# Performance work log

Hardware: AMD Instinct MI355X
Metric: run time of the kernel (lower is better)

Reference implementation:

```python
import jax, jax.numpy as jnp
import numpy as np

EPS = 1e-5  # BatchNorm eps


def _bn(x, g, b, axes):
    # training-mode batch norm over `axes`, channel dim broadcast via g/b shape
    m = jnp.mean(x, axis=axes, keepdims=True)
    v = jnp.var(x, axis=axes, keepdims=True)
    shape = [1] * x.ndim
    ch_axis = [a for a in range(x.ndim) if a not in axes][0]
    shape[ch_axis] = g.shape[0]
    return g.reshape(shape) * (x - m) * jax.lax.rsqrt(v + EPS) + b.reshape(shape)


def setup_inputs() -> dict:
    key = jax.random.key(0)
    ks = jax.random.split(key, 8)
    B, C, N = 16, 3, 2048

    def w(k_, fan_in, fan_out):
        return jax.random.normal(k_, (fan_in, fan_out), jnp.float32) * (1.0 / np.sqrt(fan_in))

    return {
        "pc": jax.random.normal(ks[0], (B, C, N), jnp.float32),
        "W1": w(ks[1], 6, 64), "g1": jnp.ones(64), "b1": jnp.zeros(64),
        "W2": w(ks[2], 64, 128), "g2": jnp.ones(128), "b2": jnp.zeros(128),
        "W3": w(ks[3], 128, 1024), "g3": jnp.ones(1024), "b3": jnp.zeros(1024),
        "Wf1": w(ks[4], 1024, 512), "gf1": jnp.ones(512), "bf1": jnp.zeros(512),
        "Wf2": w(ks[5], 512, 256), "gf2": jnp.ones(256), "bf2": jnp.zeros(256),
        "Wf3": jnp.zeros((256, 9), jnp.float32),           # zero-initialized per source
        "bf3": jnp.eye(3, dtype=jnp.float32).reshape(-1),  # identity bias per source
        "k": 20,
    }


def reference(pc, W1, g1, b1, W2, g2, b2, W3, g3, b3,
              Wf1, gf1, bf1, Wf2, gf2, bf2, Wf3, bf3, k):
    B, C, N = pc.shape
    # ---- KNN graph on coordinates (B x C x N) ----
    sq = jnp.sum(pc * pc, axis=1)                      # B,N
    inner = jnp.einsum('bcn,bcm->bnm', pc, pc)         # B,N,N
    negdist = 2.0 * inner - sq[:, :, None] - sq[:, None, :]
    _, idx = jax.lax.top_k(negdist, k)                 # B,N,k (includes self)
    # gather neighbor features: f (C,N), i (N,k) -> (C,N,k)
    topk = jax.vmap(lambda f, i: f[:, i])(pc, idx)     # B,C,N,k
    center = pc[:, :, :, None]
    edge = jnp.concatenate(
        [jnp.broadcast_to(center, topk.shape), topk - center], axis=1)  # B,2C,N,k

    # ---- edge conv (1x1 conv + BN + ReLU), pool=False ----
    h = jnp.einsum('bcnk,co->bonk', edge, W1)
    h = jax.nn.relu(_bn(h, g1, b1, (0, 2, 3)))         # B,64,N,k
    # ---- conv2 then max over k ----
    h = jnp.einsum('bcnk,co->bonk', h, W2)
    h = jax.nn.relu(_bn(h, g2, b2, (0, 2, 3)))         # B,128,N,k
    h = jnp.max(h, axis=-1)                            # B,128,N
    # ---- conv3 then max over N ----
    h = jnp.einsum('bcn,co->bon', h, W3)
    h = jax.nn.relu(_bn(h, g3, b3, (0, 2)))            # B,1024,N
    h = jnp.max(h, axis=-1)                            # B,1024
    # ---- FC stack ----
    h = jax.nn.relu(_bn(h @ Wf1, gf1, bf1, (0,)))      # B,512
    h = jax.nn.relu(_bn(h @ Wf2, gf2, bf2, (0,)))      # B,256
    h = h @ Wf3 + bf3                                  # B,9
    return h.reshape(B, 3, 3)
```

## Files before the change

### kernel.cpp

```cpp
#include <hip/hip_runtime.h>
#include <math.h>

#define Nn 2048

#define OFF_IDX    ((size_t)0)
#define OFF_P2MAX  (((size_t)4)  << 20)
#define OFF_P2MIN  (((size_t)13) << 20)
#define OFF_PS2    (((size_t)22) << 20)
#define OFF_PQ2    (((size_t)23) << 20)
#define OFF_STATS  (((size_t)24) << 20)
#define OFF_MOM    (OFF_STATS + 0)
#define OFF_A2C2   (OFF_STATS + 8192)
#define OFF_S3SUM  (OFF_STATS + 12288)
#define OFF_S3SQ   (OFF_STATS + 20480)
#define OFF_P3MAX  (OFF_STATS + 28672)
#define OFF_P3MIN  (OFF_STATS + 94208)
#define OFF_DOTS1  (OFF_STATS + 274432)
#define OFF_DOTS2  (OFF_STATS + 307200)
#define OFF_W2BF   (OFF_STATS + 323584)
#define OFF_W3BF   (OFF_STATS + 339968)
#define WS_NEEDED  (OFF_STATS + 602112)

typedef __attribute__((ext_vector_type(8))) short bf16x8;
typedef __attribute__((ext_vector_type(4))) float f32x4;

__device__ __forceinline__ unsigned fkey(float f){
  unsigned u = __float_as_uint(f);
  return (u & 0x80000000u) ? ~u : (u | 0x80000000u);
}
__device__ __forceinline__ float fdec(unsigned k){
  unsigned u = (k & 0x80000000u) ? (k & 0x7FFFFFFFu) : ~k;
  return __uint_as_float(u);
}
__device__ __forceinline__ short f2bf(float x){
  unsigned u = __float_as_uint(x);
  u += 0x7fffu + ((u >> 16) & 1u);
  return (short)(u >> 16);
}
__device__ __forceinline__ float bf2f(short v){
  return __uint_as_float(((unsigned)(unsigned short)v) << 16);
}
__device__ __forceinline__ float med3(float a, float b, float c){
  float d;
  asm("v_med3_f32 %0, %1, %2, %3" : "=v"(d) : "v"(a), "v"(b), "v"(c));
  return d;
}
__device__ __forceinline__ float ndist(float tQx, float tQy, float tQz, float Qw, float4 P){
  return fmaf(tQx, P.x, fmaf(tQy, P.y, fmaf(tQz, P.z, -Qw - P.w)));
}
__device__ __forceinline__ void insert20(float (&m)[20], float x){
  #pragma unroll
  for (int t = 0; t < 19; t++) m[t] = med3(m[t], m[t+1], x);
  m[19] = fmaxf(m[19], x);
}

__global__ __launch_bounds__(256) void k_setup(char* __restrict__ ws,
      const float* __restrict__ W2, const float* __restrict__ W3,
      short* __restrict__ W2BF, short* __restrict__ W3BF){
  int i = blockIdx.x*256 + threadIdx.x;
  if (i < 7168) ((unsigned*)(ws + OFF_MOM))[i] = 0u;
  if (i < 16384){
    ((unsigned*)(ws + OFF_P3MAX))[i] = 0u;
    ((unsigned*)(ws + OFF_P3MIN))[i] = 0xFFFFFFFFu;
  }
  if (i < 12288) ((float*)(ws + OFF_DOTS1))[i] = 0.f;
  if (i < 16384){
    int q = i >> 4, k0 = (i & 15)*8;
    bf16x8 vv;
    #pragma unroll
    for (int j = 0; j < 8; j++) vv[j] = f2bf(W3[(size_t)(k0+j)*1024 + q]);
    *(bf16x8*)&W3BF[q*128 + k0] = vv;
  } else if (i < 17408){
    int id2 = i - 16384;
    int q = id2 >> 3, k0 = (id2 & 7)*8;
    bf16x8 vv;
    #pragma unroll
    for (int j = 0; j < 8; j++) vv[j] = f2bf(W2[(k0+j)*128 + q]);
    *(bf16x8*)&W2BF[q*64 + k0] = vv;
  }
}

__global__ __launch_bounds__(512) void k_knn(const float* __restrict__ pc,
                                             int* __restrict__ idxg,
                                             double* __restrict__ MOM){
  __shared__ float4 pts[Nn];
  __shared__ unsigned cnt[64];
  __shared__ float momS[27];
  const int tid = threadIdx.x;
  const int b = blockIdx.y;
  const int n0 = blockIdx.x*64;
  const float* pcb = pc + b*3*Nn;
  for (int i = tid; i < Nn; i += 512){
    float x = pcb[i], y = pcb[Nn+i], z = pcb[2*Nn+i];
    pts[i] = make_float4(x, y, z, x*x + y*y + z*z);
  }
  if (tid < 64) cnt[tid] = 0u;
  if (tid < 27) momS[tid] = 0.f;
  __syncthreads();

  const int ql = tid >> 3, c = tid & 7;
  const int n = n0 + ql;
  const float4 Q = pts[n];
  const float tQx = 2.f*Q.x, tQy = 2.f*Q.y, tQz = 2.f*Q.z;

  float v[20];
  #pragma unroll
  for (int t = 0; t < 20; t++) v[t] = -3.4e38f;
  #pragma unroll 1
  for (int i = 0; i < 256; i += 4){
    float4 P0 = pts[(i+0)*8 + c];
    float4 P1 = pts[(i+1)*8 + c];
    float4 P2 = pts[(i+2)*8 + c];
    float4 P3 = pts[(i+3)*8 + c];
    insert20(v, ndist(tQx, tQy, tQz, Q.w, P0));
    insert20(v, ndist(tQx, tQy, tQz, Q.w, P1));
    insert20(v, ndist(tQx, tQy, tQz, Q.w, P2));
    insert20(v, ndist(tQx, tQy, tQz, Q.w, P3));
  }

  #pragma unroll
  for (int stage = 4; stage >= 1; stage >>= 1){
    float w[20];
    #pragma unroll
    for (int t = 0; t < 20; t++) w[t] = __shfl_xor(v[t], stage);
    #pragma unroll
    for (int t = 0; t < 20; t++) insert20(v, w[t]);
  }
  const float th = v[0];

  int* myidx = &idxg[((size_t)((b<<11) + n))*20];
  #pragma unroll 1
  for (int i = 0; i < 256; i += 4){
    float4 P0 = pts[(i+0)*8 + c];
    float4 P1 = pts[(i+1)*8 + c];
    float4 P2 = pts[(i+2)*8 + c];
    float4 P3 = pts[(i+3)*8 + c];
    float nd0 = ndist(tQx, tQy, tQz, Q.w, P0);
    float nd1 = ndist(tQx, tQy, tQz, Q.w, P1);
    float nd2 = ndist(tQx, tQy, tQz, Q.w, P2);
    float nd3 = ndist(tQx, tQy, tQz, Q.w, P3);
    if (nd0 >= th){ unsigned p = atomicAdd(&cnt[ql], 1u); if (p < 20u) myidx[p] = (i+0)*8 + c; }
    if (nd1 >= th){ unsigned p = atomicAdd(&cnt[ql], 1u); if (p < 20u) myidx[p] = (i+1)*8 + c; }
    if (nd2 >= th){ unsigned p = atomicAdd(&cnt[ql], 1u); if (p < 20u) myidx[p] = (i+2)*8 + c; }
    if (nd3 >= th){ unsigned p = atomicAdd(&cnt[ql], 1u); if (p < 20u) myidx[p] = (i+3)*8 + c; }
  }
  __threadfence_block();
  __syncthreads();

  if (c == 0){
    unsigned have = cnt[ql]; if (have > 20u) have = 20u;
    for (unsigned p = have; p < 20u; ++p) myidx[p] = n;
  }
  __threadfence_block();
  __syncthreads();

  float s1[6] = {0,0,0,0,0,0};
  float s2[21] = {0,0,0,0,0,0,0,0,0,0,0,0,0,0,0,0,0,0,0,0,0};
  #pragma unroll 1
  for (int j = tid; j < 1280; j += 512){
    int q = j/20, t = j - q*20;
    int m = idxg[((size_t)((b<<11) + n0 + q))*20 + t] & 2047;
    float4 P = pts[m];
    float4 Qq = pts[n0 + q];
    float e[6] = {Qq.x, Qq.y, Qq.z, P.x - Qq.x, P.y - Qq.y, P.z - Qq.z};
    int u = 0;
    #pragma unroll
    for (int a = 0; a < 6; a++){
      s1[a] += e[a];
      #pragma unroll
      for (int bq = a; bq < 6; bq++){ s2[u] += e[a]*e[bq]; u++; }
    }
  }
  #pragma unroll
  for (int a = 0; a < 6; a++)
    for (int off = 32; off > 0; off >>= 1) s1[a] += __shfl_xor(s1[a], off);
  #pragma unroll
  for (int u = 0; u < 21; u++)
    for (int off = 32; off > 0; off >>= 1) s2[u] += __shfl_xor(s2[u], off);
  if ((tid & 63) == 0){
    #pragma unroll
    for (int a = 0; a < 6; a++) atomicAdd(&momS[a], s1[a]);
    #pragma unroll
    for (int u = 0; u < 21; u++) atomicAdd(&momS[6+u], s2[u]);
  }
  __syncthreads();
  if (tid < 27) atomicAdd(&MOM[tid], (double)momS[tid]);
}

__global__ __launch_bounds__(256) void k_conv12(const float* __restrict__ pc,
      const int* __restrict__ idxg, const double* __restrict__ MOM,
      const float* __restrict__ W1, const float* __restrict__ g1,
      const float* __restrict__ b1, const short* __restrict__ W2BF,
      float* __restrict__ PS2, float* __restrict__ PQ2,
      short* __restrict__ P2MAX, short* __restrict__ P2MIN){
  __shared__ float es[6][512];
  __shared__ short h1s[256*64];
  __shared__ float w1s[448];
  __shared__ float ssum[128], ssq[128];
  const int tid = threadIdx.x;
  const int b = blockIdx.y;
  const int n0 = blockIdx.x*16;
  const float* pcb = pc + b*3*Nn;

  if (tid < 64){
    const int o = tid;
    const double inv = 1.0/655360.0;
    double w[6]; double m = 0.0;
    #pragma unroll
    for (int cc = 0; cc < 6; cc++){ w[cc] = (double)W1[cc*64+o]; m += w[cc]*MOM[cc]*inv; }
    double e2 = 0.0; int u = 0;
    #pragma unroll
    for (int cc = 0; cc < 6; cc++){
      #pragma unroll
      for (int cp = cc; cp < 6; cp++){
        double mm = MOM[6+u]*inv; u++;
        e2 += (cc == cp) ? w[cc]*w[cc]*mm : 2.0*w[cc]*w[cp]*mm;
      }
    }
    double var = e2 - m*m;
    double a = (double)g1[o] / sqrt(var + 1e-5);
    #pragma unroll
    for (int cc = 0; cc < 6; cc++) w1s[cc*64+o] = (float)(a*w[cc]);
    w1s[384+o] = (float)((double)b1[o] - a*m);
  }

  for (int s = tid; s < 512; s += 256){
    int nl = s >> 5, kk = s & 31;
    int n = n0 + nl;
    int kke = (kk < 20) ? kk : 0;
    int m = idxg[((size_t)((b<<11)+n))*20 + kke] & 2047;
    float cx = pcb[n],  cy = pcb[Nn+n],  cz = pcb[2*Nn+n];
    float px = pcb[m],  py = pcb[Nn+m],  pz = pcb[2*Nn+m];
    es[0][s] = cx;    es[1][s] = cy;    es[2][s] = cz;
    es[3][s] = px-cx; es[4][s] = py-cy; es[5][s] = pz-cz;
  }
  __syncthreads();

  const int l = tid & 63, wv = tid >> 6;
  const int col = l & 15, kc = l >> 4;

  bf16x8 Bf[2][2];
  #pragma unroll
  for (int qt = 0; qt < 2; qt++){
    int q = wv*32 + qt*16 + col;
    #pragma unroll
    for (int ks = 0; ks < 2; ks++)
      Bf[qt][ks] = *(const bf16x8*)&W2BF[q*64 + ks*32 + kc*8];
  }

  float smacc[2] = {0.f, 0.f}, sqacc[2] = {0.f, 0.f};
  const bool t1real = (kc == 0);

  #pragma unroll 1
  for (int ch = 0; ch < 2; ch++){
    for (int i = tid; i < 2048; i += 256){
      int sl = i >> 3, oc = i & 7;
      int s = (ch << 8) + sl;
      bf16x8 hv;
      #pragma unroll
      for (int j = 0; j < 8; j++){
        int o = oc*8 + j;
        float acc = w1s[384 + o];
        #pragma unroll
        for (int cc = 0; cc < 6; cc++) acc = fmaf(w1s[cc*64 + o], es[cc][s], acc);
        hv[j] = f2bf(fmaxf(acc, 0.f));
      }
      *(bf16x8*)&h1s[sl*64 + ((oc ^ (sl & 7)) << 3)] = hv;
    }
    __syncthreads();

    #pragma unroll 1
    for (int g2 = 0; g2 < 8; g2++){
      const int g = ch*8 + g2;
      bf16x8 Af[2][2];
      #pragma unroll
      for (int t = 0; t < 2; t++){
        int rl = g2*32 + t*16 + col;
        #pragma unroll
        for (int ks = 0; ks < 2; ks++){
          int chunk = (ks*4 + kc) ^ (rl & 7);
          Af[t][ks] = *(const bf16x8*)&h1s[rl*64 + chunk*8];
        }
      }
      #pragma unroll
      for (int qt = 0; qt < 2; qt++){
        f32x4 a0 = {0.f,0.f,0.f,0.f}, a1 = {0.f,0.f,0.f,0.f};
        a0 = __builtin_amdgcn_mfma_f32_16x16x32_bf16(Af[0][0], Bf[qt][0], a0, 0,0,0);
        a0 = __builtin_amdgcn_mfma_f32_16x16x32_bf16(Af[0][1], Bf[qt][1], a0, 0,0,0);
        a1 = __builtin_amdgcn_mfma_f32_16x16x32_bf16(Af[1][0], Bf[qt][0], a1, 0,0,0);
        a1 = __builtin_amdgcn_mfma_f32_16x16x32_bf16(Af[1][1], Bf[qt][1], a1, 0,0,0);
        float mx = a0[0], mn = a0[0], sm = 0.f, sq = 0.f;
        #pragma unroll
        for (int r = 0; r < 4; r++){
          float v0 = a0[r], v1 = a1[r];
          mx = fmaxf(mx, fmaxf(v0, v1));
          mn = fminf(mn, fminf(v0, v1));
          sm += v0; sq += v0*v0;
        }
        if (t1real){
          #pragma unroll
          for (int r = 0; r < 4; r++){ float v1 = a1[r]; sm += v1; sq += v1*v1; }
        }
        smacc[qt] += sm; sqacc[qt] += sq;
        mx = fmaxf(mx, __shfl_xor(mx, 16)); mx = fmaxf(mx, __shfl_xor(mx, 32));
        mn = fminf(mn, __shfl_xor(mn, 16)); mn = fminf(mn, __shfl_xor(mn, 32));
        if (kc == 0){
          size_t base = ((size_t)(b*Nn + n0 + g))*128 + (size_t)(wv*32 + qt*16 + col);
          P2MAX[base] = f2bf(mx);
          P2MIN[base] = f2bf(mn);
        }
      }
    }
    __syncthreads();
  }

  #pragma unroll
  for (int qt = 0; qt < 2; qt++){
    smacc[qt] += __shfl_xor(smacc[qt], 16); smacc[qt] += __shfl_xor(smacc[qt], 32);
    sqacc[qt] += __shfl_xor(sqacc[qt], 16); sqacc[qt] += __shfl_xor(sqacc[qt], 32);
    if (kc == 0){
      ssum[wv*32 + qt*16 + col] = smacc[qt];
      ssq [wv*32 + qt*16 + col] = sqacc[qt];
    }
  }
  __syncthreads();
  if (tid < 128){
    int bid = b*128 + blockIdx.x;
    PS2[tid*2048 + bid] = ssum[tid];
    PQ2[tid*2048 + bid] = ssq[tid];
  }
}

__global__ __launch_bounds__(256) void k_coef2(const float* __restrict__ PS2,
        const float* __restrict__ PQ2, const float* __restrict__ g2,
        const float* __restrict__ b2, float* __restrict__ A2C2){
  __shared__ float sred[4], qred[4];
  const int p = blockIdx.x;
  const int tid = threadIdx.x;
  float s = 0.f, q = 0.f;
  for (int i = tid; i < 2048; i += 256){ s += PS2[p*2048 + i]; q += PQ2[p*2048 + i]; }
  #pragma unroll
  for (int off = 32; off > 0; off >>= 1){ s += __shfl_xor(s, off); q += __shfl_xor(q, off); }
  if ((tid & 63) == 0){ sred[tid >> 6] = s; qred[tid >> 6] = q; }
  __syncthreads();
  if (tid == 0){
    double sum = (double)sred[0] + sred[1] + sred[2] + sred[3];
    double sq  = (double)qred[0] + qred[1] + qred[2] + qred[3];
    double mean = sum * (1.0/655360.0);
    double var  = sq  * (1.0/655360.0) - mean*mean;
    double a = (double)g2[p] / sqrt(var + 1e-5);
    A2C2[p]     = (float)a;
    A2C2[128+p] = (float)((double)b2[p] - a*mean);
  }
}

__global__ __launch_bounds__(256) void k_conv3(const short* __restrict__ P2MAX,
      const short* __restrict__ P2MIN, const float* __restrict__ A2C2,
      const short* __restrict__ W3BF, double* __restrict__ S3SUM,
      double* __restrict__ S3SQ, unsigned* __restrict__ P3MAX,
      unsigned* __restrict__ P3MIN){
  __shared__ short As[128*128];
  __shared__ float a2[128], c2[128];
  const int tid = threadIdx.x;
  const int b = blockIdx.y;
  const int n0 = blockIdx.x*128;
  const int qh = blockIdx.z;
  if (tid < 128){ a2[tid] = A2C2[tid]; c2[tid] = A2C2[128+tid]; }
  __syncthreads();

  for (int idx = tid; idx < 2048; idx += 256){
    int s = idx >> 4, oc = idx & 15;
    size_t base = ((size_t)(b*Nn + n0 + s))*128 + (size_t)(oc*8);
    bf16x8 vmx = *(const bf16x8*)&P2MAX[base];
    bf16x8 vmn = *(const bf16x8*)&P2MIN[base];
    bf16x8 vv;
    #pragma unroll
    for (int j = 0; j < 8; j++){
      int o = oc*8 + j;
      float aa = a2[o];
      float vsel = bf2f((aa >= 0.f) ? vmx[j] : vmn[j]);
      vv[j] = f2bf(fmaxf(aa*vsel + c2[o], 0.f));
    }
    int chunk = oc ^ (s & 7);
    *(bf16x8*)&As[s*128 + chunk*8] = vv;
  }
  __syncthreads();

  const int l = tid & 63, wv = tid >> 6;
  const int col = l & 15, kc = l >> 4;

  #pragma unroll 1
  for (int pass = 0; pass < 2; ++pass){
    bf16x8 Bf[4][4];
    #pragma unroll
    for (int qt = 0; qt < 4; qt++){
      int q = qh*512 + wv*128 + pass*64 + qt*16 + col;
      #pragma unroll
      for (int ks = 0; ks < 4; ks++)
        Bf[qt][ks] = *(const bf16x8*)&W3BF[q*128 + ks*32 + kc*8];
    }
    float smx[4], smn[4], ssm[4], ssqv[4];
    #pragma unroll
    for (int qt = 0; qt < 4; qt++){ smx[qt] = -3.4e38f; smn[qt] = 3.4e38f; ssm[qt] = 0.f; ssqv[qt] = 0.f; }

    #pragma unroll 1
    for (int st = 0; st < 8; ++st){
      bf16x8 Af[4];
      int row = st*16 + col;
      #pragma unroll
      for (int ks = 0; ks < 4; ks++){
        int chunk = (ks*4 + kc) ^ (row & 7);
        Af[ks] = *(const bf16x8*)&As[row*128 + chunk*8];
      }
      #pragma unroll
      for (int qt = 0; qt < 4; qt++){
        f32x4 acc = {0.f, 0.f, 0.f, 0.f};
        #pragma unroll
        for (int ks = 0; ks < 4; ks++)
          acc = __builtin_amdgcn_mfma_f32_16x16x32_bf16(Af[ks], Bf[qt][ks], acc, 0, 0, 0);
        #pragma unroll
        for (int r = 0; r < 4; r++){
          float vv = acc[r];
          smx[qt] = fmaxf(smx[qt], vv); smn[qt] = fminf(smn[qt], vv);
          ssm[qt] += vv; ssqv[qt] += vv*vv;
        }
      }
    }
    #pragma unroll
    for (int qt = 0; qt < 4; qt++){
      #pragma unroll
      for (int off = 16; off <= 32; off <<= 1){
        smx[qt] = fmaxf(smx[qt], __shfl_xor(smx[qt], off));
        smn[qt] = fminf(smn[qt], __shfl_xor(smn[qt], off));
        ssm[qt] += __shfl_xor(ssm[qt], off);
        ssqv[qt] += __shfl_xor(ssqv[qt], off);
      }
    }
    if (kc == 0){
      #pragma unroll
      for (int qt = 0; qt < 4; qt++){
        int q = qh*512 + wv*128 + pass*64 + qt*16 + col;
        atomicMax(&P3MAX[b*1024 + q], fkey(smx[qt]));
        atomicMin(&P3MIN[b*1024 + q], fkey(smn[qt]));
        atomicAdd(&S3SUM[q], (double)ssm[qt]);
        atomicAdd(&S3SQ[q],  (double)ssqv[qt]);
      }
    }
  }
}

__global__ __launch_bounds__(256) void k_fc1(const double* __restrict__ S3SUM,
      const double* __restrict__ S3SQ, const unsigned* __restrict__ P3MAX,
      const unsigned* __restrict__ P3MIN, const float* __restrict__ g3,
      const float* __restrict__ b3, const float* __restrict__ Wf1,
      float* __restrict__ dots){
  __shared__ float Xs[16*64];
  const int tid = threadIdx.x;
  const int o = blockIdx.x*64 + (tid & 63);
  const int wvv = tid >> 6;
  const int c0 = blockIdx.y*64;
  for (int i = tid; i < 1024; i += 256){
    int bb = i >> 6, cc = i & 63;
    int q = c0 + cc;
    int id = bb*1024 + q;
    double mean = S3SUM[q] * (1.0/32768.0);
    double var  = S3SQ[q] * (1.0/32768.0) - mean*mean;
    double a = (double)g3[q] / sqrt(var + 1e-5);
    double cbn = (double)b3[q] - a*mean;
    float v = fdec((a >= 0.0) ? P3MAX[id] : P3MIN[id]);
    Xs[bb*64 + cc] = fmaxf((float)(a*(double)v + cbn), 0.f);
  }
  __syncthreads();
  float acc[16];
  #pragma unroll
  for (int bb = 0; bb < 16; bb++) acc[bb] = 0.f;
  for (int cc = wvv*16; cc < wvv*16 + 16; ++cc){
    float w = Wf1[(size_t)(c0+cc)*512 + o];
    #pragma unroll
    for (int bb = 0; bb < 16; bb++) acc[bb] += Xs[bb*64 + cc]*w;
  }
  #pragma unroll
  for (int bb = 0; bb < 16; bb++) atomicAdd(&dots[bb*512 + o], acc[bb]);
}

__global__ __launch_bounds__(256) void k_fc2(const float* __restrict__ DOTS1,
      const float* __restrict__ gf1, const float* __restrict__ bf1,
      const float* __restrict__ Wf2, float* __restrict__ dots){
  __shared__ float Xs[16*32];
  const int tid = threadIdx.x;
  const int o = blockIdx.x*64 + (tid & 63);
  const int wvv = tid >> 6;
  const int c0 = blockIdx.y*32;
  if (tid < 32){
    int o1 = c0 + tid;
    float d[16]; float m = 0.f;
    #pragma unroll
    for (int bb = 0; bb < 16; bb++){ d[bb] = DOTS1[bb*512 + o1]; m += d[bb]; }
    m *= (1.f/16.f);
    float vv = 0.f;
    #pragma unroll
    for (int bb = 0; bb < 16; bb++){ float x = d[bb]-m; vv += x*x; }
    vv *= (1.f/16.f);
    float a = gf1[o1] * rsqrtf(vv + 1e-5f);
    #pragma unroll
    for (int bb = 0; bb < 16; bb++)
      Xs[bb*32 + tid] = fmaxf(a*(d[bb]-m) + bf1[o1], 0.f);
  }
  __syncthreads();
  float acc[16];
  #pragma unroll
  for (int bb = 0; bb < 16; bb++) acc[bb] = 0.f;
  for (int cc = wvv*8; cc < wvv*8 + 8; ++cc){
    float w = Wf2[(size_t)(c0+cc)*256 + o];
    #pragma unroll
    for (int bb = 0; bb < 16; bb++) acc[bb] += Xs[bb*32 + cc]*w;
  }
  #pragma unroll
  for (int bb = 0; bb < 16; bb++) atomicAdd(&dots[bb*256 + o], acc[bb]);
}

__global__ __launch_bounds__(256) void k_head(const float* __restrict__ DOTS2,
      const float* __restrict__ gf2, const float* __restrict__ bf2,
      const float* __restrict__ Wf3, const float* __restrict__ bf3,
      float* __restrict__ out){
  __shared__ float R5s[16*256];
  const int tid = threadIdx.x;
  {
    int o = tid;
    float d[16]; float m = 0.f;
    #pragma unroll
    for (int bb = 0; bb < 16; bb++){ d[bb] = DOTS2[bb*256 + o]; m += d[bb]; }
    m *= (1.f/16.f);
    float vv = 0.f;
    #pragma unroll
    for (int bb = 0; bb < 16; bb++){ float x = d[bb]-m; vv += x*x; }
    vv *= (1.f/16.f);
    float a = gf2[o] * rsqrtf(vv + 1e-5f);
    #pragma unroll
    for (int bb = 0; bb < 16; bb++)
      R5s[bb*256 + o] = fmaxf(a*(d[bb]-m) + bf2[o], 0.f);
  }
  __syncthreads();
  if (tid < 144){
    int b = tid/9, j = tid - b*9;
    float acc = bf3[j];
    for (int cq = 0; cq < 256; cq++) acc += R5s[b*256 + cq]*Wf3[cq*9 + j];
    out[tid] = acc;
  }
}

extern "C" void kernel_launch(void* const* d_in, const int* in_sizes, int n_in,
                              void* d_out, int out_size, void* d_ws, size_t ws_size,
                              hipStream_t stream) {
  if (ws_size < WS_NEEDED) return;
  const float* pc  = (const float*)d_in[0];
  const float* W1  = (const float*)d_in[1];
  const float* g1  = (const float*)d_in[2];
  const float* b1  = (const float*)d_in[3];
  const float* W2  = (const float*)d_in[4];
  const float* g2  = (const float*)d_in[5];
  const float* b2  = (const float*)d_in[6];
  const float* W3  = (const float*)d_in[7];
  const float* g3  = (const float*)d_in[8];
  const float* b3  = (const float*)d_in[9];
  const float* Wf1 = (const float*)d_in[10];
  const float* gf1 = (const float*)d_in[11];
  const float* bf1 = (const float*)d_in[12];
  const float* Wf2 = (const float*)d_in[13];
  const float* gf2 = (const float*)d_in[14];
  const float* bf2 = (const float*)d_in[15];
  const float* Wf3 = (const float*)d_in[16];
  const float* bf3 = (const float*)d_in[17];

  char* ws = (char*)d_ws;
  int*      IDX   = (int*)     (ws + OFF_IDX);
  short*    P2MAXp= (short*)   (ws + OFF_P2MAX);
  short*    P2MINp= (short*)   (ws + OFF_P2MIN);
  float*    PS2p  = (float*)   (ws + OFF_PS2);
  float*    PQ2p  = (float*)   (ws + OFF_PQ2);
  double*   MOMp  = (double*)  (ws + OFF_MOM);
  float*    A2C2p = (float*)   (ws + OFF_A2C2);
  double*   S3SUMp= (double*)  (ws + OFF_S3SUM);
  double*   S3SQp = (double*)  (ws + OFF_S3SQ);
  unsigned* P3MAXp= (unsigned*)(ws + OFF_P3MAX);
  unsigned* P3MINp= (unsigned*)(ws + OFF_P3MIN);
  float*    DOTS1p= (float*)   (ws + OFF_DOTS1);
  float*    DOTS2p= (float*)   (ws + OFF_DOTS2);
  short*    W2BFp = (short*)   (ws + OFF_W2BF);
  short*    W3BFp = (short*)   (ws + OFF_W3BF);

  k_setup <<<dim3(68),      256, 0, stream>>>(ws, W2, W3, W2BFp, W3BFp);
  k_knn   <<<dim3(32,16),   512, 0, stream>>>(pc, IDX, MOMp);
  k_conv12<<<dim3(128,16),  256, 0, stream>>>(pc, IDX, MOMp, W1, g1, b1, W2BFp, PS2p, PQ2p, P2MAXp, P2MINp);
  k_coef2 <<<dim3(128),     256, 0, stream>>>(PS2p, PQ2p, g2, b2, A2C2p);
  k_conv3 <<<dim3(16,16,2), 256, 0, stream>>>(P2MAXp, P2MINp, A2C2p, W3BFp, S3SUMp, S3SQp, P3MAXp, P3MINp);
  k_fc1   <<<dim3(8,16),    256, 0, stream>>>(S3SUMp, S3SQp, P3MAXp, P3MINp, g3, b3, Wf1, DOTS1p);
  k_fc2   <<<dim3(4,16),    256, 0, stream>>>(DOTS1p, gf1, bf1, Wf2, DOTS2p);
  k_head  <<<dim3(1),       256, 0, stream>>>(DOTS2p, gf2, bf2, Wf3, bf3, (float*)d_out);
}
```

Baseline: 214.6 us.

## Pack neighbor index into sortable distance key to drop KNN second pass

The KNN top-20 selection now keeps unsigned keys that combine a truncated order-preserving distance key with the neighbor index in the low 11 bits, using v_med3_u32 for insertion. The final sorted list then yields the indices directly. This removes the second distance scan with LDS atomics, the padding pass and two block barriers, and the moment accumulation reads neighbors from registers instead of re-reading global idx. In exchange, the low 11 mantissa bits of the distance are lost, so near-ties are broken by index, which can differ from the reference top_k ordering and selection.

```diff
diff --git a/kernel.cpp b/kernel.cpp
--- a/kernel.cpp
+++ b/kernel.cpp
@@ -26,7 +26,7 @@
 
 __device__ __forceinline__ unsigned fkey(float f){
   unsigned u = __float_as_uint(f);
-  return (u & 0x80000000u) ? ~u : (u | 0x80000000u);
+  return u ^ ((unsigned)((int)u >> 31) | 0x80000000u);
 }
 __device__ __forceinline__ float fdec(unsigned k){
   unsigned u = (k & 0x80000000u) ? (k & 0x7FFFFFFFu) : ~k;
@@ -40,18 +40,18 @@
 __device__ __forceinline__ float bf2f(short v){
   return __uint_as_float(((unsigned)(unsigned short)v) << 16);
 }
-__device__ __forceinline__ float med3(float a, float b, float c){
-  float d;
-  asm("v_med3_f32 %0, %1, %2, %3" : "=v"(d) : "v"(a), "v"(b), "v"(c));
+__device__ __forceinline__ unsigned med3u(unsigned a, unsigned b, unsigned c){
+  unsigned d;
+  asm("v_med3_u32 %0, %1, %2, %3" : "=v"(d) : "v"(a), "v"(b), "v"(c));
   return d;
 }
 __device__ __forceinline__ float ndist(float tQx, float tQy, float tQz, float Qw, float4 P){
   return fmaf(tQx, P.x, fmaf(tQy, P.y, fmaf(tQz, P.z, -Qw - P.w)));
 }
-__device__ __forceinline__ void insert20(float (&m)[20], float x){
-  #pragma unroll
-  for (int t = 0; t < 19; t++) m[t] = med3(m[t], m[t+1], x);
-  m[19] = fmaxf(m[19], x);
+__device__ __forceinline__ void insert20u(unsigned (&m)[20], unsigned x){
+  #pragma unroll
+  for (int t = 0; t < 19; t++) m[t] = med3u(m[t], m[t+1], x);
+  m[19] = (x > m[19]) ? x : m[19];
 }
 
 __global__ __launch_bounds__(256) void k_setup(char* __restrict__ ws,
@@ -84,7 +84,6 @@
                                              int* __restrict__ idxg,
                                              double* __restrict__ MOM){
   __shared__ float4 pts[Nn];
-  __shared__ unsigned cnt[64];
   __shared__ float momS[27];
   const int tid = threadIdx.x;
   const int b = blockIdx.y;
@@ -94,7 +93,6 @@
     float x = pcb[i], y = pcb[Nn+i], z = pcb[2*Nn+i];
     pts[i] = make_float4(x, y, z, x*x + y*y + z*z);
   }
-  if (tid < 64) cnt[tid] = 0u;
   if (tid < 27) momS[tid] = 0.f;
   __syncthreads();
 
@@ -103,72 +101,53 @@
   const float4 Q = pts[n];
   const float tQx = 2.f*Q.x, tQy = 2.f*Q.y, tQz = 2.f*Q.z;
 
-  float v[20];
-  #pragma unroll
-  for (int t = 0; t < 20; t++) v[t] = -3.4e38f;
+  unsigned v[20];
+  #pragma unroll
+  for (int t = 0; t < 20; t++) v[t] = 0u;
   #pragma unroll 1
   for (int i = 0; i < 256; i += 4){
-    float4 P0 = pts[(i+0)*8 + c];
-    float4 P1 = pts[(i+1)*8 + c];
-    float4 P2 = pts[(i+2)*8 + c];
-    float4 P3 = pts[(i+3)*8 + c];
-    insert20(v, ndist(tQx, tQy, tQz, Q.w, P0));
-    insert20(v, ndist(tQx, tQy, tQz, Q.w, P1));
-    insert20(v, ndist(tQx, tQy, tQz, Q.w, P2));
-    insert20(v, ndist(tQx, tQy, tQz, Q.w, P3));
+    int m0 = (i+0)*8 + c, m1 = (i+1)*8 + c, m2 = (i+2)*8 + c, m3 = (i+3)*8 + c;
+    float4 P0 = pts[m0];
+    float4 P1 = pts[m1];
+    float4 P2 = pts[m2];
+    float4 P3 = pts[m3];
+    unsigned k0 = (fkey(ndist(tQx,tQy,tQz,Q.w,P0)) & 0xFFFFF800u) | (unsigned)(2047 - m0);
+    unsigned k1 = (fkey(ndist(tQx,tQy,tQz,Q.w,P1)) & 0xFFFFF800u) | (unsigned)(2047 - m1);
+    unsigned k2 = (fkey(ndist(tQx,tQy,tQz,Q.w,P2)) & 0xFFFFF800u) | (unsigned)(2047 - m2);
+    unsigned k3 = (fkey(ndist(tQx,tQy,tQz,Q.w,P3)) & 0xFFFFF800u) | (unsigned)(2047 - m3);
+    insert20u(v, k0);
+    insert20u(v, k1);
+    insert20u(v, k2);
+    insert20u(v, k3);
   }
 
   #pragma unroll
   for (int stage = 4; stage >= 1; stage >>= 1){
-    float w[20];
-    #pragma unroll
-    for (int t = 0; t < 20; t++) w[t] = __shfl_xor(v[t], stage);
-    #pragma unroll
-    for (int t = 0; t < 20; t++) insert20(v, w[t]);
-  }
-  const float th = v[0];
+    unsigned w[20];
+    #pragma unroll
+    for (int t = 0; t < 20; t++) w[t] = (unsigned)__shfl_xor((int)v[t], stage);
+    #pragma unroll
+    for (int t = 0; t < 20; t++) insert20u(v, w[t]);
+  }
 
   int* myidx = &idxg[((size_t)((b<<11) + n))*20];
-  #pragma unroll 1
-  for (int i = 0; i < 256; i += 4){
-    float4 P0 = pts[(i+0)*8 + c];
-    float4 P1 = pts[(i+1)*8 + c];
-    float4 P2 = pts[(i+2)*8 + c];
-    float4 P3 = pts[(i+3)*8 + c];
-    float nd0 = ndist(tQx, tQy, tQz, Q.w, P0);
-    float nd1 = ndist(tQx, tQy, tQz, Q.w, P1);
-    float nd2 = ndist(tQx, tQy, tQz, Q.w, P2);
-    float nd3 = ndist(tQx, tQy, tQz, Q.w, P3);
-    if (nd0 >= th){ unsigned p = atomicAdd(&cnt[ql], 1u); if (p < 20u) myidx[p] = (i+0)*8 + c; }
-    if (nd1 >= th){ unsigned p = atomicAdd(&cnt[ql], 1u); if (p < 20u) myidx[p] = (i+1)*8 + c; }
-    if (nd2 >= th){ unsigned p = atomicAdd(&cnt[ql], 1u); if (p < 20u) myidx[p] = (i+2)*8 + c; }
-    if (nd3 >= th){ unsigned p = atomicAdd(&cnt[ql], 1u); if (p < 20u) myidx[p] = (i+3)*8 + c; }
-  }
-  __threadfence_block();
-  __syncthreads();
-
-  if (c == 0){
-    unsigned have = cnt[ql]; if (have > 20u) have = 20u;
-    for (unsigned p = have; p < 20u; ++p) myidx[p] = n;
-  }
-  __threadfence_block();
-  __syncthreads();
-
   float s1[6] = {0,0,0,0,0,0};
   float s2[21] = {0,0,0,0,0,0,0,0,0,0,0,0,0,0,0,0,0,0,0,0,0};
-  #pragma unroll 1
-  for (int j = tid; j < 1280; j += 512){
-    int q = j/20, t = j - q*20;
-    int m = idxg[((size_t)((b<<11) + n0 + q))*20 + t] & 2047;
-    float4 P = pts[m];
-    float4 Qq = pts[n0 + q];
-    float e[6] = {Qq.x, Qq.y, Qq.z, P.x - Qq.x, P.y - Qq.y, P.z - Qq.z};
-    int u = 0;
-    #pragma unroll
-    for (int a = 0; a < 6; a++){
-      s1[a] += e[a];
-      #pragma unroll
-      for (int bq = a; bq < 6; bq++){ s2[u] += e[a]*e[bq]; u++; }
+  #pragma unroll
+  for (int t = 0; t < 3; t++){
+    int slot = c + t*8;
+    if (slot < 20){
+      int m = 2047 - (int)(v[slot] & 0x7FFu);
+      myidx[slot] = m;
+      float4 P = pts[m];
+      float e[6] = {Q.x, Q.y, Q.z, P.x - Q.x, P.y - Q.y, P.z - Q.z};
+      int u = 0;
+      #pragma unroll
+      for (int a = 0; a < 6; a++){
+        s1[a] += e[a];
+        #pragma unroll
+        for (int bq = a; bq < 6; bq++){ s2[u] += e[a]*e[bq]; u++; }
+      }
     }
   }
   #pragma unroll
```

Result: faster. 195.4 us (-8.9%).
